# Optimization experiments

Measured on AMD Instinct MI355X. Metric: run time of the kernel, lower is better.

## Reference

```python
import jax, jax.numpy as jnp
import numpy as np

GAP = 7  # average_gap from init
B, T = 4096, 8192


def setup_inputs() -> dict:
    key = jax.random.key(0)
    # prices must be nonzero (Percentage divides by previous price)
    x = jax.random.uniform(key, (B, T), dtype=jnp.float32) + 0.5
    return {"x": x}


def reference(x):
    g = GAP
    prev = x[:, :-1]                               # (B, T-1)
    # Delta then Percentage: (x[t+1]-x[t]) / x[t]
    p = (x[:, 1:] - prev) / prev                   # (B, T-1)
    # Norm: divide by per-sample max(|max|, |min|)
    scale = jnp.maximum(jnp.max(p, axis=1), jnp.abs(jnp.min(p, axis=1)))  # (B,)
    pn = p / scale[:, None]                        # (B, T-1)
    # MovingAverage via cumulative sum (replaces per-step loop)
    c = jnp.cumsum(pn, axis=1)                     # (B, T-1)
    win_sum = c[:, g - 1:] - jnp.pad(c, ((0, 0), (1, 0)))[:, :-g]  # (B, T-g)
    ma = win_sum / g                               # (B, T-g)
    # final concat along feature axis
    return jnp.stack([ma, x[:, :-g]], axis=2)      # (B, T-g, 2)
```

## Files before the change

kernel.cpp:

```cpp
#include <hip/hip_runtime.h>


constexpr int T_LEN = 8192;
constexpr int GAP_  = 7;
constexpr int OUTW  = T_LEN - GAP_;
constexpr int NP    = T_LEN - 1;
constexpr int NTHR  = 256;
constexpr int PAIRS = 4092;

__global__ __launch_bounds__(NTHR)
void forex_prep_kernel(const float* __restrict__ x, float* __restrict__ out,
                       int n_rows) {
    const int row = blockIdx.x;
    if (row >= n_rows) return;
    const int t = threadIdx.x;

    __shared__ float xs[T_LEN];
    __shared__ float red[NTHR / 64];

    const float* __restrict__ xr = x + (size_t)row * T_LEN;

#pragma unroll
    for (int i = 0; i < T_LEN / (4 * NTHR); ++i) {
        const int e = (i * NTHR + t) * 4;
        const float4 v = *reinterpret_cast<const float4*>(xr + e);
        *reinterpret_cast<float4*>(xs + e) = v;
    }
    __syncthreads();

    float m = 0.0f;
#pragma unroll
    for (int i = 0; i < T_LEN / NTHR; ++i) {
        const int k = i * NTHR + t;
        if (k < NP) {
            const float pk = fmaf(xs[k + 1], __builtin_amdgcn_rcpf(xs[k]), -1.0f);
            m = fmaxf(m, fabsf(pk));
        }
    }
#pragma unroll
    for (int off = 32; off > 0; off >>= 1)
        m = fmaxf(m, __shfl_xor(m, off, 64));
    if ((t & 63) == 0) red[t >> 6] = m;
    __syncthreads();
    const float scale = fmaxf(fmaxf(red[0], red[1]), fmaxf(red[2], red[3]));
    const float inv = __builtin_amdgcn_rcpf(scale * (float)GAP_);

    const int s = row & 1;
    float* __restrict__ ob = out + (size_t)row * (OUTW * 2);

#pragma unroll
    for (int i = 0; i < 16; ++i) {
        const int u = i * NTHR + t;
        if (u < PAIRS) {
            const int j = s + 2 * u;
            float xv[9];
#pragma unroll
            for (int e = 0; e < 9; ++e) xv[e] = xs[j + e];
            float p[8];
#pragma unroll
            for (int e = 0; e < 8; ++e)
                p[e] = fmaf(xv[e + 1], __builtin_amdgcn_rcpf(xv[e]), -1.0f);
            const float w0 = p[0] + p[1] + p[2] + p[3] + p[4] + p[5] + p[6];
            const float w1 = w0 - p[0] + p[7];
            *reinterpret_cast<float4*>(ob + 2 * j) =
                make_float4(w0 * inv, xv[0], w1 * inv, xv[1]);
        }
    }

    if (t == 0) {
        const int j = s ? 0 : (OUTW - 1);
        float w = 0.0f;
#pragma unroll
        for (int e = 0; e < GAP_; ++e)
            w += fmaf(xs[j + e + 1], __builtin_amdgcn_rcpf(xs[j + e]), -1.0f);
        *reinterpret_cast<float2*>(ob + 2 * j) = make_float2(w * inv, xs[j]);
    }
}

extern "C" void kernel_launch(void* const* d_in, const int* in_sizes, int n_in,
                              void* d_out, int out_size, void* d_ws, size_t ws_size,
                              hipStream_t stream) {
    const float* x = (const float*)d_in[0];
    float* out = (float*)d_out;
    const int n_rows = in_sizes[0] / T_LEN;
    dim3 grid(n_rows), block(NTHR);
    hipLaunchKernelGGL(forex_prep_kernel, grid, block, 0, stream, x, out, n_rows);
}
```

Baseline: 83.33 us.

## Compute max from registers during load and process four outputs per thread with vector LDS reads

The max-abs reduction now runs on the float4 values already in registers during the global load, using a wavefront shuffle for the cross-lane neighbor and a small fixup for wave boundaries. This removes a second full pass over shared memory. The output phase now handles four consecutive outputs per thread, reading shared memory with float4/float2 loads and producing the sliding window incrementally, so fewer scalar LDS reads and reciprocals are needed per output. The cost is more registers, parity-dependent branches, and more complex boundary logic.

```diff
diff --git a/kernel.cpp b/kernel.cpp
--- a/kernel.cpp
+++ b/kernel.cpp
@@ -4,9 +4,8 @@
 constexpr int T_LEN = 8192;
 constexpr int GAP_  = 7;
 constexpr int OUTW  = T_LEN - GAP_;
-constexpr int NP    = T_LEN - 1;
 constexpr int NTHR  = 256;
-constexpr int PAIRS = 4092;
+constexpr int QUADS = 2046;
 
 __global__ __launch_bounds__(NTHR)
 void forex_prep_kernel(const float* __restrict__ x, float* __restrict__ out,
@@ -20,22 +19,31 @@
 
     const float* __restrict__ xr = x + (size_t)row * T_LEN;
 
+    float4 v[8];
 #pragma unroll
-    for (int i = 0; i < T_LEN / (4 * NTHR); ++i) {
+    for (int i = 0; i < 8; ++i) {
         const int e = (i * NTHR + t) * 4;
-        const float4 v = *reinterpret_cast<const float4*>(xr + e);
-        *reinterpret_cast<float4*>(xs + e) = v;
+        v[i] = *reinterpret_cast<const float4*>(xr + e);
+        *reinterpret_cast<float4*>(xs + e) = v[i];
+    }
+    float m = 0.0f;
+#pragma unroll
+    for (int i = 0; i < 8; ++i) {
+        const float xn = __shfl_down(v[i].x, 1, 64);
+        const float p0 = fmaf(v[i].y, __builtin_amdgcn_rcpf(v[i].x), -1.0f);
+        const float p1 = fmaf(v[i].z, __builtin_amdgcn_rcpf(v[i].y), -1.0f);
+        const float p2 = fmaf(v[i].w, __builtin_amdgcn_rcpf(v[i].z), -1.0f);
+        m = fmaxf(m, fmaxf(fabsf(p0), fmaxf(fabsf(p1), fabsf(p2))));
+        if ((t & 63) != 63) {
+            const float p3 = fmaf(xn, __builtin_amdgcn_rcpf(v[i].w), -1.0f);
+            m = fmaxf(m, fabsf(p3));
+        }
     }
     __syncthreads();
-
-    float m = 0.0f;
-#pragma unroll
-    for (int i = 0; i < T_LEN / NTHR; ++i) {
-        const int k = i * NTHR + t;
-        if (k < NP) {
-            const float pk = fmaf(xs[k + 1], __builtin_amdgcn_rcpf(xs[k]), -1.0f);
-            m = fmaxf(m, fabsf(pk));
-        }
+    if (t < 31) {
+        const int k = 256 * t + 255;
+        const float pk = fmaf(xs[k + 1], __builtin_amdgcn_rcpf(xs[k]), -1.0f);
+        m = fmaxf(m, fabsf(pk));
     }
 #pragma unroll
     for (int off = 32; off > 0; off >>= 1)
@@ -47,23 +55,43 @@
 
     const int s = row & 1;
     float* __restrict__ ob = out + (size_t)row * (OUTW * 2);
+    const float4* xs4 = reinterpret_cast<const float4*>(xs);
+    const float2* xs2 = reinterpret_cast<const float2*>(xs);
 
 #pragma unroll
-    for (int i = 0; i < 16; ++i) {
-        const int u = i * NTHR + t;
-        if (u < PAIRS) {
-            const int j = s + 2 * u;
-            float xv[9];
+    for (int i = 0; i < 8; ++i) {
+        const int g = i * NTHR + t;
+        if (g < QUADS) {
+            float xv[11];
+            if (s == 0) {
+                const float4 a0 = xs4[g];
+                const float4 a1 = xs4[g + 1];
+                const float2 b  = xs2[2 * g + 4];
+                const float  c  = xs[4 * g + 10];
+                xv[0]=a0.x; xv[1]=a0.y; xv[2]=a0.z; xv[3]=a0.w;
+                xv[4]=a1.x; xv[5]=a1.y; xv[6]=a1.z; xv[7]=a1.w;
+                xv[8]=b.x;  xv[9]=b.y;  xv[10]=c;
+            } else {
+                const float4 a0 = xs4[g];
+                const float4 a1 = xs4[g + 1];
+                const float4 a2 = xs4[g + 2];
+                xv[0]=a0.y; xv[1]=a0.z; xv[2]=a0.w;
+                xv[3]=a1.x; xv[4]=a1.y; xv[5]=a1.z; xv[6]=a1.w;
+                xv[7]=a2.x; xv[8]=a2.y; xv[9]=a2.z; xv[10]=a2.w;
+            }
+            float p[10];
 #pragma unroll
-            for (int e = 0; e < 9; ++e) xv[e] = xs[j + e];
-            float p[8];
-#pragma unroll
-            for (int e = 0; e < 8; ++e)
+            for (int e = 0; e < 10; ++e)
                 p[e] = fmaf(xv[e + 1], __builtin_amdgcn_rcpf(xv[e]), -1.0f);
-            const float w0 = p[0] + p[1] + p[2] + p[3] + p[4] + p[5] + p[6];
+            const float w0 = ((p[0]+p[1]) + (p[2]+p[3])) + ((p[4]+p[5]) + p[6]);
             const float w1 = w0 - p[0] + p[7];
-            *reinterpret_cast<float4*>(ob + 2 * j) =
+            const float w2 = w1 - p[1] + p[8];
+            const float w3 = w2 - p[2] + p[9];
+            const int j2 = 2 * (s + 4 * g);
+            *reinterpret_cast<float4*>(ob + j2) =
                 make_float4(w0 * inv, xv[0], w1 * inv, xv[1]);
+            *reinterpret_cast<float4*>(ob + j2 + 4) =
+                make_float4(w2 * inv, xv[2], w3 * inv, xv[3]);
         }
     }
 
```

Result: slower. 87.34 us (+4.8%).
